# Performance work log

Measured on AMD Instinct MI355X. Metric: run time of the kernel, lower is better.

## Reference

```python
import jax, jax.numpy as jnp
import numpy as np

D_LATENT = 128
WIDTH = 64
MODES = 32
N_LAYERS = 4
N_INST = 8
LIFT_L = 64   # lift_shape = (width, 64)
B = 128
OUT_LEN = 4096
EPS = 1e-5


def _gelu(x):
    return jax.nn.gelu(x, approximate=False)  # torch nn.GELU default = exact erf


def setup_inputs() -> dict:
    key = jax.random.key(0)
    ks = jax.random.split(key, 16)
    n = lambda k, shape, s=0.02: (s * jax.random.normal(k, shape)).astype(jnp.float32)
    spec_scale = 1.0 / (WIDTH * WIDTH)
    return {
        "z": jax.random.normal(ks[0], (B, D_LATENT), dtype=jnp.float32),
        "instrument_params": jax.random.normal(ks[1], (B, N_INST), dtype=jnp.float32),
        "lift_w": n(ks[2], (D_LATENT, WIDTH * LIFT_L)),
        "lift_b": jnp.zeros((WIDTH * LIFT_L,), jnp.float32),
        "inst_w1": n(ks[3], (N_INST, WIDTH), 0.3),
        "inst_b1": jnp.zeros((WIDTH,), jnp.float32),
        "inst_w2": n(ks[4], (WIDTH, WIDTH), 0.1),
        "inst_b2": jnp.zeros((WIDTH,), jnp.float32),
        "spec_w": (spec_scale * jax.random.normal(ks[5], (N_LAYERS, WIDTH, WIDTH, MODES, 2))).astype(jnp.float32),
        "pw_w": n(ks[6], (N_LAYERS, WIDTH, WIDTH), 0.1),   # (layer, out, in)
        "pw_b": jnp.zeros((N_LAYERS, WIDTH), jnp.float32),
        "proj_w1": n(ks[7], (2 * WIDTH, WIDTH), 0.1),      # (out, in)
        "proj_b1": jnp.zeros((2 * WIDTH,), jnp.float32),
        "proj_w2": n(ks[8], (1, 2 * WIDTH), 0.1),
        "proj_b2": jnp.zeros((1,), jnp.float32),
        "out_len": OUT_LEN,
    }


def _interp_linear(x, out_len):
    # torch F.interpolate(mode='linear', align_corners=False)
    in_len = x.shape[-1]
    src = jnp.clip((jnp.arange(out_len, dtype=x.dtype) + 0.5) * (in_len / out_len) - 0.5, 0.0, in_len - 1)
    i0 = jnp.floor(src).astype(jnp.int32)
    i1 = jnp.minimum(i0 + 1, in_len - 1)
    w = src - i0.astype(x.dtype)
    return x[..., i0] * (1.0 - w) + x[..., i1] * w


def _spectral_conv(x, w):
    # x: (B, C, L) real; w: (C_in, C_out, modes, 2)
    L = x.shape[-1]
    xf = jnp.fft.rfft(x, axis=-1)                 # (B, C, L//2+1) complex64
    xr = jnp.real(xf[:, :, :MODES])
    xi = jnp.imag(xf[:, :, :MODES])
    wr, wi = w[..., 0], w[..., 1]
    out_r = jnp.einsum('bim,iom->bom', xr, wr) - jnp.einsum('bim,iom->bom', xi, wi)
    out_i = jnp.einsum('bim,iom->bom', xr, wi) + jnp.einsum('bim,iom->bom', xi, wr)
    n_freq = L // 2 + 1
    of = (out_r + 1j * out_i).astype(xf.dtype)
    of = jnp.pad(of, ((0, 0), (0, 0), (0, n_freq - MODES)))
    return jnp.fft.irfft(of, n=L, axis=-1)


def reference(z, instrument_params, lift_w, lift_b, inst_w1, inst_b1, inst_w2, inst_b2,
              spec_w, pw_w, pw_b, proj_w1, proj_b1, proj_w2, proj_b2, out_len):
    Bz = z.shape[0]
    x = (z @ lift_w + lift_b).reshape(Bz, WIDTH, LIFT_L)
    x = _interp_linear(x, out_len)                              # (B, W, L)
    cond = _gelu(instrument_params @ inst_w1 + inst_b1) @ inst_w2 + inst_b2
    x = x + cond[:, :, None]
    for l in range(N_LAYERS):
        x1 = _spectral_conv(x, spec_w[l])
        x2 = jnp.einsum('bil,oi->bol', x, pw_w[l]) + pw_b[l][None, :, None]
        h = x1 + x2
        mu = h.mean(axis=-1, keepdims=True)
        var = h.var(axis=-1, keepdims=True)                     # biased, like InstanceNorm1d
        x = _gelu((h - mu) * jax.lax.rsqrt(var + EPS))
    h = _gelu(jnp.einsum('bil,oi->bol', x, proj_w1) + proj_b1[None, :, None])
    out = jnp.einsum('bil,oi->bol', h, proj_w2) + proj_b2[None, :, None]
    return out[:, 0, :]                                         # (B, out_len)
```

## Files before the change

### kernel.cpp

```cpp
#include <hip/hip_runtime.h>
#include <math.h>


typedef _Float16 half8 __attribute__((ext_vector_type(8)));
typedef __attribute__((ext_vector_type(4))) float fx4;

__device__ __forceinline__ float gelu_f(float x){
    float u = x*x;
    float a = x * fmaf(-0.1029443f, u, -2.3022083f);
    float e = exp2f(a);
    float r = __builtin_amdgcn_rcpf(1.0f + e);
    return x * r;
}
__device__ __forceinline__ unsigned short f2h(float f){
    union { _Float16 h; unsigned short u; } c;
    c.h = (_Float16)f;
    return c.u;
}
__device__ __forceinline__ float h2f(unsigned short u){
    union { unsigned short u; _Float16 h; } c;
    c.u = u;
    return (float)c.h;
}

static const size_t OFF_XH    = 0;
static const size_t OFF_XT    = 16777216;
static const size_t OFF_TABB  = 33554432;
static const size_t OFF_TABT  = 33685504;
static const size_t OFF_MAH   = 33816576;
static const size_t OFF_PWWH  = 34078720;
static const size_t OFF_W1H   = 34086912;
static const size_t OFF_COND  = 34091008;
static const size_t OFF_STATS = 34099200;
static const size_t OFF_DFTP  = 34115584;
static const size_t OFF_X0    = 38309888;

__global__ void k_tab(unsigned short* __restrict__ tabB, unsigned short* __restrict__ tabT,
                      const float* __restrict__ pww, unsigned short* __restrict__ pwwh,
                      const float* __restrict__ pj1w, unsigned short* __restrict__ w1h){
    int t = blockIdx.x*256 + threadIdx.x;
    if (t < 16384) pwwh[t] = f2h(pww[t]);
    if (t < 8192)  w1h[t]  = f2h(pj1w[t]);
    int m2 = t >> 12, n = t & 4095;
    int m = m2 & 31;
    int r = (m*n) & 4095;
    int r2 = (r >= 2048) ? (r - 4096) : r;
    float a = (float)r2 * 1.5339807878856412e-3f;
    float v = (m2 >= 32) ? sinf(a) : cosf(a);
    tabB[(size_t)m2*4096 + n] = f2h(v);
    tabT[(size_t)n*64 + m2]   = f2h(v * 0.015625f);
}

__global__ __launch_bounds__(64) void k_cond(const float* __restrict__ instp,
        const float* __restrict__ w1, const float* __restrict__ b1,
        const float* __restrict__ w2, const float* __restrict__ b2,
        float* __restrict__ cond){
    int b = blockIdx.x, tid = threadIdx.x;
    __shared__ float ipl[8];
    __shared__ float tl[64];
    if (tid < 8) ipl[tid] = instp[b*8 + tid];
    __syncthreads();
    float s = b1[tid];
    #pragma unroll
    for (int k = 0; k < 8; ++k) s = fmaf(ipl[k], w1[k*64 + tid], s);
    tl[tid] = gelu_f(s);
    __syncthreads();
    float c = b2[tid];
    #pragma unroll 8
    for (int j = 0; j < 64; ++j) c = fmaf(tl[j], w2[j*64 + tid], c);
    cond[b*64 + tid] = c;
}

__global__ __launch_bounds__(256) void k_liftc(const float* __restrict__ z,
        const float* __restrict__ lw, const float* __restrict__ lb,
        const float* __restrict__ cond, float* __restrict__ x0){
    int b = blockIdx.x, q = blockIdx.y;
    int t = threadIdx.x;
    __shared__ float zl[128];
    if (t < 128) zl[t] = z[b*128 + t];
    __syncthreads();
    #pragma unroll
    for (int i = 0; i < 4; ++i){
        int e = q*1024 + i*256 + t;
        float s = lb[e];
        #pragma unroll 8
        for (int d = 0; d < 128; ++d)
            s = fmaf(zl[d], lw[(size_t)d*4096 + e], s);
        x0[(size_t)b*4096 + e] = s + cond[b*64 + (e >> 6)];
    }
}

template<int MODE, int DODFT>
__global__ __launch_bounds__(256) void k_prep(
        const unsigned short* __restrict__ xhp, const float* __restrict__ statsr,
        const unsigned short* __restrict__ tabB, const float* __restrict__ x0,
        unsigned short* __restrict__ xT, float* __restrict__ dftp)
{
    int b = blockIdx.x, ng = blockIdx.y;
    int t = threadIdx.x;
    int w = t >> 6, lane = t & 63;
    int lrow = lane & 15, g = lane >> 4;
    __shared__ __align__(16) unsigned short xl[2][4096];
    __shared__ float xs[(MODE == 2) ? 65*64 : 1];
    int co = t >> 2, nq = t & 3;
    float mu = 0.f, rs = 1.f;
    if (MODE == 1){
        float2 sr = *(const float2*)(statsr + (size_t)(b*64+co)*2);
        mu = sr.x * (1.f/4096.f);
        float var = fmaf(sr.y, 1.f/4096.f, -mu*mu);
        rs = rsqrtf(var + 1e-5f);
    }
    if (MODE == 2){
        const float* xb0 = x0 + (size_t)b*4096;
        #pragma unroll
        for (int i = 0; i < 16; ++i){
            int idx = i*256 + t;
            xs[(idx >> 6)*65 + (idx & 63)] = xb0[idx];
        }
        __syncthreads();
    }
    fx4 acc[4];
    #pragma unroll
    for (int i = 0; i < 4; ++i) acc[i] = (fx4){0.f,0.f,0.f,0.f};

    const unsigned short* hrow = xhp + ((size_t)(b*64+co))*4096 + ng*512 + nq*16;
    unsigned short* xtbase = xT + ((size_t)b*4096 + (size_t)ng*512)*64;

    uint4 cA, cB;
    if (MODE == 1){ cA = *(const uint4*)(hrow); cB = *(const uint4*)(hrow + 8); }
    for (int it = 0; it < 8; ++it){
        int n0 = ng*512 + it*64;
        char* xb = (char*)(&xl[it & 1][0]);
        uint4 nA, nB;
        if (MODE == 1 && it < 7){
            nA = *(const uint4*)(hrow + (it+1)*64);
            nB = *(const uint4*)(hrow + (it+1)*64 + 8);
        }
        unsigned int pk[8];
        if (MODE == 1){
            unsigned int hu[8] = {cA.x,cA.y,cA.z,cA.w,cB.x,cB.y,cB.z,cB.w};
            #pragma unroll
            for (int i = 0; i < 8; ++i){
                float f0 = h2f((unsigned short)(hu[i] & 0xFFFFu));
                float f1 = h2f((unsigned short)(hu[i] >> 16));
                f0 = gelu_f((f0 - mu)*rs);
                f1 = gelu_f((f1 - mu)*rs);
                pk[i] = (unsigned int)f2h(f0) | ((unsigned int)f2h(f1) << 16);
            }
        } else {
            const float* xr = xs + co*65;
            #pragma unroll
            for (int i = 0; i < 8; ++i){
                float v[2];
                #pragma unroll
                for (int q = 0; q < 2; ++q){
                    int n = n0 + nq*16 + i*2 + q;
                    float src = (n + 0.5f)*0.015625f - 0.5f;
                    src = fminf(fmaxf(src, 0.0f), 63.0f);
                    int i0 = (int)src;
                    int i1 = (i0 + 1 > 63) ? 63 : (i0 + 1);
                    float wt = src - (float)i0;
                    v[q] = xr[i0] + wt*(xr[i1] - xr[i0]);
                }
                pk[i] = (unsigned int)f2h(v[0]) | ((unsigned int)f2h(v[1]) << 16);
            }
        }
        unsigned int base = (unsigned int)co*128 + (unsigned int)nq*32;
        unsigned int sw = (unsigned int)((co & 7) << 4);
        *(uint4*)(xb + ((base +  0) ^ sw)) = make_uint4(pk[0],pk[1],pk[2],pk[3]);
        *(uint4*)(xb + ((base + 16) ^ sw)) = make_uint4(pk[4],pk[5],pk[6],pk[7]);
        __syncthreads();

        if (DODFT){
            int m0 = w*16;
            #pragma unroll
            for (int ks = 0; ks < 2; ++ks){
                int kk = ks*32 + g*8;
                half8 af = *(const half8*)(tabB + (size_t)(m0 + lrow)*4096 + n0 + kk);
                #pragma unroll
                for (int ct = 0; ct < 4; ++ct){
                    int row = ct*16 + lrow;
                    unsigned int ba = ((unsigned int)row*128 + (unsigned int)kk*2)
                                      ^ (unsigned int)((row & 7) << 4);
                    half8 bf = *(const half8*)(xb + ba);
                    acc[ct] = __builtin_amdgcn_mfma_f32_16x16x32_f16(af, bf, acc[ct], 0, 0, 0);
                }
            }
        }
        {
            int n = t & 63, coq = t >> 6;
            unsigned int opk[8];
            #pragma unroll
            for (int i = 0; i < 8; ++i){
                int r0 = coq*16 + 2*i, r1 = r0 + 1;
                unsigned int a0 = ((unsigned int)r0*128 + (unsigned int)n*2)
                                  ^ (unsigned int)((r0 & 7) << 4);
                unsigned int a1 = ((unsigned int)r1*128 + (unsigned int)n*2)
                                  ^ (unsigned int)((r1 & 7) << 4);
                unsigned short v0 = *(const unsigned short*)(xb + a0);
                unsigned short v1 = *(const unsigned short*)(xb + a1);
                opk[i] = (unsigned int)v0 | ((unsigned int)v1 << 16);
            }
            unsigned short* dst = xtbase + (size_t)(it*64 + n)*64 + coq*16;
            *(uint4*)dst       = make_uint4(opk[0],opk[1],opk[2],opk[3]);
            *(uint4*)(dst + 8) = make_uint4(opk[4],opk[5],opk[6],opk[7]);
        }
        if (MODE == 1 && it < 7){ cA = nA; cB = nB; }
    }
    if (DODFT){
        int m0 = w*16;
        #pragma unroll
        for (int ct = 0; ct < 4; ++ct){
            float4 v = make_float4(acc[ct][0], acc[ct][1], acc[ct][2], acc[ct][3]);
            *(float4*)(dftp + ((size_t)(b*8+ng)*64 + ct*16 + lrow)*64 + m0 + g*4) = v;
        }
    }
}

__global__ __launch_bounds__(256) void k_mix(const float* __restrict__ dftp,
        const float* __restrict__ specw, unsigned short* __restrict__ mah,
        float* __restrict__ statsr, int l){
    int b = blockIdx.x, coq = blockIdx.y, t = threadIdx.x;
    __shared__ float xm[64*64];
    if (t < 128) statsr[b*128 + t] = 0.f;
    const float* dp = dftp + (size_t)b*8*4096;
    #pragma unroll
    for (int i = 0; i < 4; ++i){
        int e = i*1024 + t*4;
        float4 s = make_float4(0.f,0.f,0.f,0.f);
        #pragma unroll
        for (int ng = 0; ng < 8; ++ng){
            float4 v = *(const float4*)(dp + (size_t)ng*4096 + e);
            s.x += v.x; s.y += v.y; s.z += v.z; s.w += v.w;
        }
        if (e & 32){ s.x = -s.x; s.y = -s.y; s.z = -s.z; s.w = -s.w; }
        *(float4*)(xm + e) = s;
    }
    __syncthreads();
    int mq = t & 3, ciq = (t >> 2) & 3, co_l = t >> 4;
    int co = coq*16 + co_l;
    float yr[8] = {0,0,0,0,0,0,0,0}, yi[8] = {0,0,0,0,0,0,0,0};
    const float* wbase = specw + (size_t)l*262144 + (size_t)co*64 + mq*16;
    #pragma unroll 4
    for (int cil = 0; cil < 16; ++cil){
        int ci = ciq*16 + cil;
        const float* wp = wbase + (size_t)ci*4096;
        float4 w0 = *(const float4*)(wp);
        float4 w1v = *(const float4*)(wp + 4);
        float4 w2v = *(const float4*)(wp + 8);
        float4 w3v = *(const float4*)(wp + 12);
        const float* xc = xm + ci*64 + mq*8;
        float4 r0 = *(const float4*)(xc);
        float4 r1 = *(const float4*)(xc + 4);
        float4 i0 = *(const float4*)(xc + 32);
        float4 i1 = *(const float4*)(xc + 36);
        float wr[8] = {w0.x,w0.z,w1v.x,w1v.z,w2v.x,w2v.z,w3v.x,w3v.z};
        float wi[8] = {w0.y,w0.w,w1v.y,w1v.w,w2v.y,w2v.w,w3v.y,w3v.w};
        float xr[8] = {r0.x,r0.y,r0.z,r0.w,r1.x,r1.y,r1.z,r1.w};
        float xi[8] = {i0.x,i0.y,i0.z,i0.w,i1.x,i1.y,i1.z,i1.w};
        #pragma unroll
        for (int mm = 0; mm < 8; ++mm){
            yr[mm] = fmaf(xr[mm], wr[mm], fmaf(-xi[mm], wi[mm], yr[mm]));
            yi[mm] = fmaf(xr[mm], wi[mm], fmaf( xi[mm], wr[mm], yi[mm]));
        }
    }
    #pragma unroll
    for (int mm = 0; mm < 8; ++mm){
        yr[mm] += __shfl_xor(yr[mm], 4); yr[mm] += __shfl_xor(yr[mm], 8);
        yi[mm] += __shfl_xor(yi[mm], 4); yi[mm] += __shfl_xor(yi[mm], 8);
    }
    if (ciq == 0){
        unsigned short* mb = mah + (size_t)(b*64 + co)*64;
        unsigned int pr[4], pi[4];
        #pragma unroll
        for (int p = 0; p < 4; ++p){
            int m0 = mq*8 + 2*p;
            float s0 = (m0 == 0) ? 0.015625f : 0.03125f;
            pr[p] = (unsigned int)f2h(s0*yr[2*p]) | ((unsigned int)f2h(0.03125f*yr[2*p+1]) << 16);
            pi[p] = (unsigned int)f2h(-0.03125f*yi[2*p]) | ((unsigned int)f2h(-0.03125f*yi[2*p+1]) << 16);
        }
        *(uint4*)(mb + mq*8)      = make_uint4(pr[0],pr[1],pr[2],pr[3]);
        *(uint4*)(mb + 32 + mq*8) = make_uint4(pi[0],pi[1],pi[2],pi[3]);
    }
}

__global__ __launch_bounds__(256, 2) void k_pass3(
        const unsigned short* __restrict__ xT, const unsigned short* __restrict__ tabT,
        const unsigned short* __restrict__ pwwh, const float* __restrict__ pwb,
        const unsigned short* __restrict__ mah, unsigned short* __restrict__ xh,
        float* __restrict__ statsr, int lay)
{
    int b = blockIdx.x, ntg = blockIdx.y;
    int t = threadIdx.x, w = t >> 6, lane = t & 63;
    int lrow = lane & 15, g = lane >> 4;
    int nsl = ntg*256 + w*64;

    half8 A[4][4];
    #pragma unroll
    for (int nt = 0; nt < 4; ++nt){
        int n = nsl + nt*16 + lrow;
        #pragma unroll
        for (int ks = 0; ks < 4; ++ks){
            int k = ks*32 + g*8;
            const unsigned short* src = (k < 64)
                ? (xT   + ((size_t)b*4096 + n)*64 + k)
                : (tabT + (size_t)n*64 + (k - 64));
            A[nt][ks] = *(const half8*)src;
        }
    }
    half8 Bv[4][4];
    #pragma unroll
    for (int cot = 0; cot < 4; ++cot){
        int co = cot*16 + lrow;
        #pragma unroll
        for (int ks = 0; ks < 4; ++ks){
            int k = ks*32 + g*8;
            const unsigned short* src = (k < 64)
                ? (pwwh + ((size_t)lay*64 + co)*64 + k)
                : (mah  + ((size_t)b*64 + co)*64 + (k - 64));
            Bv[cot][ks] = *(const half8*)src;
        }
    }
    fx4 acc[4][4];
    #pragma unroll
    for (int i = 0; i < 4; ++i)
        #pragma unroll
        for (int j = 0; j < 4; ++j) acc[i][j] = (fx4){0.f,0.f,0.f,0.f};

    #pragma unroll
    for (int ks = 0; ks < 4; ++ks)
        #pragma unroll
        for (int nt = 0; nt < 4; ++nt)
            #pragma unroll
            for (int cot = 0; cot < 4; ++cot)
                acc[nt][cot] = __builtin_amdgcn_mfma_f32_16x16x32_f16(A[nt][ks], Bv[cot][ks], acc[nt][cot], 0, 0, 0);

    float sS[4] = {0,0,0,0}, sQ[4] = {0,0,0,0};
    #pragma unroll
    for (int cot = 0; cot < 4; ++cot){
        int co = cot*16 + lrow;
        float pb = pwb[lay*64 + co];
        unsigned short* hr = xh + ((size_t)(b*64+co))*4096;
        #pragma unroll
        for (int nt = 0; nt < 4; ++nt){
            float h0 = acc[nt][cot][0] + pb;
            float h1 = acc[nt][cot][1] + pb;
            float h2 = acc[nt][cot][2] + pb;
            float h3 = acc[nt][cot][3] + pb;
            uint2 pk;
            pk.x = (unsigned int)f2h(h0) | ((unsigned int)f2h(h1) << 16);
            pk.y = (unsigned int)f2h(h2) | ((unsigned int)f2h(h3) << 16);
            *(uint2*)(hr + nsl + nt*16 + g*4) = pk;
            sS[cot] += (h0 + h1) + (h2 + h3);
            float q = h0*h0;
            q = fmaf(h1, h1, q); q = fmaf(h2, h2, q); q = fmaf(h3, h3, q);
            sQ[cot] += q;
        }
    }
    __shared__ float sred[2][4][64];
    #pragma unroll
    for (int cot = 0; cot < 4; ++cot){
        float s = sS[cot], q = sQ[cot];
        s += __shfl_xor(s, 16); q += __shfl_xor(q, 16);
        s += __shfl_xor(s, 32); q += __shfl_xor(q, 32);
        if (g == 0){
            sred[0][w][cot*16 + lrow] = s;
            sred[1][w][cot*16 + lrow] = q;
        }
    }
    __syncthreads();
    if (t < 64){
        float S = 0.f, Q = 0.f;
        #pragma unroll
        for (int ww = 0; ww < 4; ++ww){ S += sred[0][ww][t]; Q += sred[1][ww][t]; }
        atomicAdd(statsr + (size_t)(b*64+t)*2,     S);
        atomicAdd(statsr + (size_t)(b*64+t)*2 + 1, Q);
    }
}

__global__ __launch_bounds__(512) void k_proj(
        const unsigned short* __restrict__ xT, const unsigned short* __restrict__ w1h,
        const float* __restrict__ b1, const float* __restrict__ w2,
        const float* __restrict__ b2, float* __restrict__ out)
{
    int b = blockIdx.x, ntg = blockIdx.y;
    int t = threadIdx.x, w = t >> 6, lane = t & 63;
    int lrow = lane & 15, g = lane >> 4;
    int o2h = w & 1, nq = w >> 1;
    int nb = ntg*512 + nq*128;

    half8 A[4][2];
    #pragma unroll
    for (int ot = 0; ot < 4; ++ot)
        #pragma unroll
        for (int ks = 0; ks < 2; ++ks)
            A[ot][ks] = *(const half8*)(w1h + (size_t)(o2h*64 + ot*16 + lrow)*64 + ks*32 + g*8);
    float bb[16], wv[16];
    #pragma unroll
    for (int ot = 0; ot < 4; ++ot)
        #pragma unroll
        for (int j = 0; j < 4; ++j){
            int o2 = o2h*64 + ot*16 + g*4 + j;
            bb[ot*4+j] = b1[o2];
            wv[ot*4+j] = w2[o2];
        }
    __shared__ float sred[4][8][2][16];
    for (int tl = 0; tl < 8; ++tl){
        int n = nb + tl*16 + lrow;
        fx4 acc[4];
        #pragma unroll
        for (int i = 0; i < 4; ++i) acc[i] = (fx4){0.f,0.f,0.f,0.f};
        #pragma unroll
        for (int ks = 0; ks < 2; ++ks){
            half8 bf = *(const half8*)(xT + ((size_t)b*4096 + n)*64 + ks*32 + g*8);
            #pragma unroll
            for (int ot = 0; ot < 4; ++ot)
                acc[ot] = __builtin_amdgcn_mfma_f32_16x16x32_f16(A[ot][ks], bf, acc[ot], 0, 0, 0);
        }
        float p = 0.f;
        #pragma unroll
        for (int ot = 0; ot < 4; ++ot)
            #pragma unroll
            for (int j = 0; j < 4; ++j)
                p = fmaf(wv[ot*4+j], gelu_f(acc[ot][j] + bb[ot*4+j]), p);
        p += __shfl_xor(p, 16); p += __shfl_xor(p, 32);
        if (lane < 16) sred[nq][tl][o2h][lane] = p;
    }
    __syncthreads();
    {
        int cl = t & 15, tlf = (t >> 4) & 7, nqf = t >> 7;
        out[(size_t)b*4096 + ntg*512 + t] =
            sred[nqf][tlf][0][cl] + sred[nqf][tlf][1][cl] + b2[0];
    }
}

extern "C" void kernel_launch(void* const* d_in, const int* in_sizes, int n_in,
                              void* d_out, int out_size, void* d_ws, size_t ws_size,
                              hipStream_t stream) {
    (void)in_sizes; (void)n_in; (void)out_size; (void)ws_size;
    const float* z      = (const float*)d_in[0];
    const float* instp  = (const float*)d_in[1];
    const float* lift_w = (const float*)d_in[2];
    const float* lift_b = (const float*)d_in[3];
    const float* iw1    = (const float*)d_in[4];
    const float* ib1    = (const float*)d_in[5];
    const float* iw2    = (const float*)d_in[6];
    const float* ib2    = (const float*)d_in[7];
    const float* specw  = (const float*)d_in[8];
    const float* pww    = (const float*)d_in[9];
    const float* pwb    = (const float*)d_in[10];
    const float* pj1w   = (const float*)d_in[11];
    const float* pj1b   = (const float*)d_in[12];
    const float* pj2w   = (const float*)d_in[13];
    const float* pj2b   = (const float*)d_in[14];

    float* ws = (float*)d_ws;
    unsigned short* xh    = (unsigned short*)(ws + OFF_XH);
    unsigned short* xT    = (unsigned short*)(ws + OFF_XT);
    unsigned short* tabB  = (unsigned short*)(ws + OFF_TABB);
    unsigned short* tabT  = (unsigned short*)(ws + OFF_TABT);
    unsigned short* mah   = (unsigned short*)(ws + OFF_MAH);
    unsigned short* pwwh  = (unsigned short*)(ws + OFF_PWWH);
    unsigned short* w1h   = (unsigned short*)(ws + OFF_W1H);
    float* cond   = ws + OFF_COND;
    float* statsr = ws + OFF_STATS;
    float* dftp   = ws + OFF_DFTP;
    float* x0     = ws + OFF_X0;
    float* out    = (float*)d_out;

    k_tab  <<<dim3(1024),  dim3(256), 0, stream>>>(tabB, tabT, pww, pwwh, pj1w, w1h);
    k_cond <<<dim3(128),   dim3(64),  0, stream>>>(instp, iw1, ib1, iw2, ib2, cond);
    k_liftc<<<dim3(128,4), dim3(256), 0, stream>>>(z, lift_w, lift_b, cond, x0);

    for (int l = 0; l < 4; ++l){
        if (l == 0)
            k_prep<2,1><<<dim3(128,8), dim3(256), 0, stream>>>(xh, statsr, tabB, x0, xT, dftp);
        else
            k_prep<1,1><<<dim3(128,8), dim3(256), 0, stream>>>(xh, statsr, tabB, x0, xT, dftp);
        k_mix  <<<dim3(128,4),  dim3(256), 0, stream>>>(dftp, specw, mah, statsr, l);
        k_pass3<<<dim3(128,16), dim3(256), 0, stream>>>(xT, tabT, pwwh, pwb, mah, xh, statsr, l);
    }
    k_prep<1,0><<<dim3(128,8), dim3(256), 0, stream>>>(xh, statsr, tabB, x0, xT, dftp);
    k_proj    <<<dim3(128,8),  dim3(512), 0, stream>>>(xT, w1h, pj1b, pj2w, pj2b, out);
}
```

Baseline: 468.2 us.

## Restructure pass3 waves into channel halves with streamed A fragments

k_pass3 now splits each block's four waves into two output-channel halves and two column ranges. Each wave keeps only 2 B-fragment sets resident and streams A fragments per k-step over four 64-column sub-slices, instead of holding all 16 A and 16 B fragments at once. This cuts register pressure, so launch bounds rise to 4 blocks per SM and the grid halves to 8 column groups of 512. The trade-off is that A tiles are loaded twice, once per channel-half wave, and there are fewer blocks in total.

```diff
diff --git a/kernel.cpp b/kernel.cpp
--- a/kernel.cpp
+++ b/kernel.cpp
@@ -284,7 +284,7 @@
     }
 }
 
-__global__ __launch_bounds__(256, 2) void k_pass3(
+__global__ __launch_bounds__(256, 4) void k_pass3(
         const unsigned short* __restrict__ xT, const unsigned short* __restrict__ tabT,
         const unsigned short* __restrict__ pwwh, const float* __restrict__ pwb,
         const unsigned short* __restrict__ mah, unsigned short* __restrict__ xh,
@@ -293,25 +293,13 @@
     int b = blockIdx.x, ntg = blockIdx.y;
     int t = threadIdx.x, w = t >> 6, lane = t & 63;
     int lrow = lane & 15, g = lane >> 4;
-    int nsl = ntg*256 + w*64;
-
-    half8 A[4][4];
-    #pragma unroll
-    for (int nt = 0; nt < 4; ++nt){
-        int n = nsl + nt*16 + lrow;
-        #pragma unroll
-        for (int ks = 0; ks < 4; ++ks){
-            int k = ks*32 + g*8;
-            const unsigned short* src = (k < 64)
-                ? (xT   + ((size_t)b*4096 + n)*64 + k)
-                : (tabT + (size_t)n*64 + (k - 64));
-            A[nt][ks] = *(const half8*)src;
-        }
-    }
-    half8 Bv[4][4];
-    #pragma unroll
-    for (int cot = 0; cot < 4; ++cot){
-        int co = cot*16 + lrow;
+    int wc = w & 1, wn = w >> 1;
+    int nwave = ntg*512 + wn*256;
+
+    half8 Bv[2][4];
+    #pragma unroll
+    for (int cot = 0; cot < 2; ++cot){
+        int co = wc*32 + cot*16 + lrow;
         #pragma unroll
         for (int ks = 0; ks < 4; ++ks){
             int k = ks*32 + g*8;
@@ -321,45 +309,63 @@
             Bv[cot][ks] = *(const half8*)src;
         }
     }
-    fx4 acc[4][4];
-    #pragma unroll
-    for (int i = 0; i < 4; ++i)
-        #pragma unroll
-        for (int j = 0; j < 4; ++j) acc[i][j] = (fx4){0.f,0.f,0.f,0.f};
-
-    #pragma unroll
-    for (int ks = 0; ks < 4; ++ks)
-        #pragma unroll
-        for (int nt = 0; nt < 4; ++nt)
-            #pragma unroll
-            for (int cot = 0; cot < 4; ++cot)
-                acc[nt][cot] = __builtin_amdgcn_mfma_f32_16x16x32_f16(A[nt][ks], Bv[cot][ks], acc[nt][cot], 0, 0, 0);
-
-    float sS[4] = {0,0,0,0}, sQ[4] = {0,0,0,0};
-    #pragma unroll
-    for (int cot = 0; cot < 4; ++cot){
-        int co = cot*16 + lrow;
-        float pb = pwb[lay*64 + co];
-        unsigned short* hr = xh + ((size_t)(b*64+co))*4096;
-        #pragma unroll
-        for (int nt = 0; nt < 4; ++nt){
-            float h0 = acc[nt][cot][0] + pb;
-            float h1 = acc[nt][cot][1] + pb;
-            float h2 = acc[nt][cot][2] + pb;
-            float h3 = acc[nt][cot][3] + pb;
-            uint2 pk;
-            pk.x = (unsigned int)f2h(h0) | ((unsigned int)f2h(h1) << 16);
-            pk.y = (unsigned int)f2h(h2) | ((unsigned int)f2h(h3) << 16);
-            *(uint2*)(hr + nsl + nt*16 + g*4) = pk;
-            sS[cot] += (h0 + h1) + (h2 + h3);
-            float q = h0*h0;
-            q = fmaf(h1, h1, q); q = fmaf(h2, h2, q); q = fmaf(h3, h3, q);
-            sQ[cot] += q;
-        }
-    }
-    __shared__ float sred[2][4][64];
-    #pragma unroll
-    for (int cot = 0; cot < 4; ++cot){
+    float pb[2];
+    pb[0] = pwb[lay*64 + wc*32 + lrow];
+    pb[1] = pwb[lay*64 + wc*32 + 16 + lrow];
+
+    float sS[2] = {0.f, 0.f}, sQ[2] = {0.f, 0.f};
+
+    #pragma unroll
+    for (int s = 0; s < 4; ++s){
+        int nsl = nwave + s*64;
+        fx4 acc[4][2];
+        #pragma unroll
+        for (int i = 0; i < 4; ++i){
+            acc[i][0] = (fx4){0.f,0.f,0.f,0.f};
+            acc[i][1] = (fx4){0.f,0.f,0.f,0.f};
+        }
+        #pragma unroll
+        for (int ks = 0; ks < 4; ++ks){
+            int k = ks*32 + g*8;
+            half8 Af[4];
+            #pragma unroll
+            for (int nt = 0; nt < 4; ++nt){
+                int n = nsl + nt*16 + lrow;
+                const unsigned short* src = (k < 64)
+                    ? (xT   + ((size_t)b*4096 + n)*64 + k)
+                    : (tabT + (size_t)n*64 + (k - 64));
+                Af[nt] = *(const half8*)src;
+            }
+            #pragma unroll
+            for (int nt = 0; nt < 4; ++nt){
+                acc[nt][0] = __builtin_amdgcn_mfma_f32_16x16x32_f16(Af[nt], Bv[0][ks], acc[nt][0], 0, 0, 0);
+                acc[nt][1] = __builtin_amdgcn_mfma_f32_16x16x32_f16(Af[nt], Bv[1][ks], acc[nt][1], 0, 0, 0);
+            }
+        }
+        #pragma unroll
+        for (int cot = 0; cot < 2; ++cot){
+            int co = wc*32 + cot*16 + lrow;
+            unsigned short* hr = xh + ((size_t)(b*64+co))*4096;
+            #pragma unroll
+            for (int nt = 0; nt < 4; ++nt){
+                float h0 = acc[nt][cot][0] + pb[cot];
+                float h1 = acc[nt][cot][1] + pb[cot];
+                float h2 = acc[nt][cot][2] + pb[cot];
+                float h3 = acc[nt][cot][3] + pb[cot];
+                uint2 pk;
+                pk.x = (unsigned int)f2h(h0) | ((unsigned int)f2h(h1) << 16);
+                pk.y = (unsigned int)f2h(h2) | ((unsigned int)f2h(h3) << 16);
+                *(uint2*)(hr + nsl + nt*16 + g*4) = pk;
+                sS[cot] += (h0 + h1) + (h2 + h3);
+                float q = h0*h0;
+                q = fmaf(h1, h1, q); q = fmaf(h2, h2, q); q = fmaf(h3, h3, q);
+                sQ[cot] += q;
+            }
+        }
+    }
+    __shared__ float sred[2][4][32];
+    #pragma unroll
+    for (int cot = 0; cot < 2; ++cot){
         float s = sS[cot], q = sQ[cot];
         s += __shfl_xor(s, 16); q += __shfl_xor(q, 16);
         s += __shfl_xor(s, 32); q += __shfl_xor(q, 32);
@@ -370,9 +376,9 @@
     }
     __syncthreads();
     if (t < 64){
-        float S = 0.f, Q = 0.f;
-        #pragma unroll
-        for (int ww = 0; ww < 4; ++ww){ S += sred[0][ww][t]; Q += sred[1][ww][t]; }
+        int wcx = t >> 5, cl = t & 31;
+        float S = sred[0][wcx][cl] + sred[0][2 + wcx][cl];
+        float Q = sred[1][wcx][cl] + sred[1][2 + wcx][cl];
         atomicAdd(statsr + (size_t)(b*64+t)*2,     S);
         atomicAdd(statsr + (size_t)(b*64+t)*2 + 1, Q);
     }
@@ -477,8 +483,8 @@
             k_prep<2,1><<<dim3(128,8), dim3(256), 0, stream>>>(xh, statsr, tabB, x0, xT, dftp);
         else
             k_prep<1,1><<<dim3(128,8), dim3(256), 0, stream>>>(xh, statsr, tabB, x0, xT, dftp);
-        k_mix  <<<dim3(128,4),  dim3(256), 0, stream>>>(dftp, specw, mah, statsr, l);
-        k_pass3<<<dim3(128,16), dim3(256), 0, stream>>>(xT, tabT, pwwh, pwb, mah, xh, statsr, l);
+        k_mix  <<<dim3(128,4), dim3(256), 0, stream>>>(dftp, specw, mah, statsr, l);
+        k_pass3<<<dim3(128,8), dim3(256), 0, stream>>>(xT, tabT, pwwh, pwb, mah, xh, statsr, l);
     }
     k_prep<1,0><<<dim3(128,8), dim3(256), 0, stream>>>(xh, statsr, tabB, x0, xT, dftp);
     k_proj    <<<dim3(128,8),  dim3(512), 0, stream>>>(xT, w1h, pj1b, pj2w, pj2b, out);
```

Result: slower. 509.1 us (+8.7%).
